# Kernel tuning notes

Hardware: AMD Instinct MI355X
Metric: run time of the kernel (lower is better)

## Reference

```python
import jax, jax.numpy as jnp
import numpy as np

# ---- constants matching init opt ----
SQRT_FRAGS = 8
N_PATCH = SQRT_FRAGS * SQRT_FRAGS  # 64
TH1_INIT = 0.85
PATCH_MEAN = 0.1
MORPH = 5          # morphology_size (odd -> same-size pooling)
STEP = 5e-5
FRAME_PATCHES = np.array([0, 1, 2, 3, 4, 5, 6, 7, 8, 15, 16, 23, 24, 31, 32, 39,
                          40, 47, 48, 55, 56, 57, 58, 59, 60, 61, 62, 63])
H = W = 3072


def setup_inputs() -> dict:
    key = jax.random.key(0)
    x = jax.random.uniform(key, (1, 1, H, W), dtype=jnp.float32)
    return {"x": x}


def _frac_above(p, th):
    # mean of where(p > th, 1, 0)
    return jnp.mean((p > th).astype(jnp.float32))


def _find_thresholds(patches):
    """Sequential per-patch threshold search with th1 carried across patches
    (faithful to the stateful self.th1 in the torch module).
    patches: (64, ph, pw). Returns per-patch final threshold (64,)."""
    f_bias = jnp.zeros((N_PATCH,), jnp.float32).at[jnp.asarray(FRAME_PATCHES)].set(0.05)

    def per_patch(th, inp):
        p, fb = inp
        lo_tgt = PATCH_MEAN + 0.02 - fb   # loop 1: while frac < lo_tgt: th -= STEP
        hi_tgt = PATCH_MEAN - 0.02 - fb   # loop 2: while frac > hi_tgt: th += STEP
        th = jax.lax.while_loop(lambda t: _frac_above(p, t) < lo_tgt,
                                lambda t: t - STEP, th)
        th = jax.lax.while_loop(lambda t: _frac_above(p, t) > hi_tgt,
                                lambda t: t + STEP, th)
        return th, th

    _, ths = jax.lax.scan(per_patch, jnp.float32(TH1_INIT), (patches, f_bias))
    return ths


def _maxpool(x, k=MORPH):
    # PyTorch MaxPool2d(k, stride=1, padding=k//2) pads with -inf -> same size
    pad = k // 2
    return jax.lax.reduce_window(
        x, -jnp.inf, jax.lax.max,
        window_dimensions=(1, 1, k, k), window_strides=(1, 1, 1, 1),
        padding=[(0, 0), (0, 0), (pad, pad), (pad, pad)])


def reference(x):
    N, c, h, w = x.shape
    ph, pw = h // SQRT_FRAGS, w // SQRT_FRAGS
    # unfold with kernel=stride=ph -> non-overlapping patches, row-major order
    patches = (x[0, 0]
               .reshape(SQRT_FRAGS, ph, SQRT_FRAGS, pw)
               .transpose(0, 2, 1, 3)
               .reshape(N_PATCH, ph, pw))
    ths = _find_thresholds(patches)
    binary = (patches > ths[:, None, None]).astype(jnp.float32)
    # fold back to full image
    img = (binary
           .reshape(SQRT_FRAGS, SQRT_FRAGS, ph, pw)
           .transpose(0, 2, 1, 3)
           .reshape(1, 1, h, w))
    # morphological close: maxpool then minpool (minpool = -maxpool(-x))
    out = -_maxpool(-_maxpool(img))
    return out
```

## Files before the change

### kernel.cpp

```cpp
#include <hip/hip_runtime.h>
#include <stdint.h>

constexpr int IMG     = 3072;
constexpr int NPIX    = IMG * IMG;
constexpr int PH      = 384;
constexpr int NPATCH  = 64;
constexpr int NSLICE  = 8;
constexpr int SROWS   = PH / NSLICE;
constexpr int WPR     = IMG / 32;
constexpr uint32_t KEY_LO = 0x3F000000u;
constexpr uint32_t STEPU = 839u;
constexpr uint32_t G0 = KEY_LO + 704u;
constexpr int NB = 9999;
constexpr int CH = (NB + 255) / 256;

constexpr int TR = 24;
constexpr int TC = 24;
constexpr int GR = IMG / TR;
constexpr int GC = WPR / TC;
constexpr int BROWS  = TR + 8;
constexpr int BWORDS = TC + 4;
constexpr int DROWS  = TR + 4;
constexpr int DWORDS = TC + 2;

constexpr size_t OFF_THS  = 0;
constexpr size_t OFF_PRIV = 512;

__global__ __launch_bounds__(256) void k_hist(const float* __restrict__ x,
                                              uint32_t* __restrict__ priv) {
    __shared__ uint32_t hist[NB];
    const int p = blockIdx.x >> 3, s = blockIdx.x & 7;
    const int t = threadIdx.x;
    const int pr = p >> 3, pc = p & 7;
    const float* base = x + (size_t)(pr * PH + s * SROWS) * IMG + pc * PH;

    for (int i = t; i < NB; i += 256) hist[i] = 0;
    __syncthreads();

    constexpr int NF4 = SROWS * (PH / 4);
    for (int i = t; i < NF4; i += 256) {
        int r = i / 96, c = i - r * 96;
        float4 v = *reinterpret_cast<const float4*>(base + (size_t)r * IMG + c * 4);
        float vals[4] = {v.x, v.y, v.z, v.w};
#pragma unroll
        for (int k = 0; k < 4; ++k) {
            uint32_t key = __float_as_uint(vals[k]);
            if (key > G0) {
                uint32_t idx = (key - KEY_LO + 134u) / 839u;
                if (idx > (uint32_t)(NB - 1)) idx = NB - 1;
                atomicAdd(&hist[idx], 1u);
            }
        }
    }
    __syncthreads();
    uint32_t* out = priv + (size_t)blockIdx.x * NB;
    for (int i = t; i < NB; i += 256) out[i] = hist[i];
}

__global__ __launch_bounds__(256) void k_scan(const uint32_t* __restrict__ priv,
                                              float* __restrict__ ths) {
    __shared__ uint32_t h[NB];
    __shared__ uint32_t csum[256];
    __shared__ uint32_t after[256];
    __shared__ int best_s[256];
    const int p = blockIdx.x, t = threadIdx.x;
    for (int i = t; i < NB; i += 256) {
        uint32_t sum = 0;
#pragma unroll
        for (int b = 0; b < NSLICE; ++b)
            sum += priv[(size_t)(p * NSLICE + b) * NB + i];
        h[i] = sum;
    }
    __syncthreads();

    const int lo = t * CH;
    const int hi = (lo + CH < NB) ? lo + CH : NB;
    uint32_t s = 0;
    for (int i = lo; i < hi; ++i) s += h[i];
    csum[t] = s;
    __syncthreads();
    if (t == 0) {
        uint32_t acc = 0;
        for (int u = 255; u >= 0; --u) { after[u] = acc; acc += csum[u]; }
    }
    __syncthreads();

    const int pr = p >> 3, pc = p & 7;
    const bool frame = (pr == 0 || pr == 7 || pc == 0 || pc == 7);
    const float hi_t = 0.08f - (frame ? 0.05f : 0.0f);
    int d = (int)((double)hi_t * 147456.0);
    while ((float)(d + 1) / 147456.0f <= hi_t) ++d;
    while (d > 0 && (float)d / 147456.0f > hi_t) --d;
    const uint32_t Chi = (uint32_t)d;

    uint32_t run = after[t];
    int best = 0x7FFFFFFF;
    for (int i = hi - 1; i >= lo; --i) {
        run += h[i];
        if (i >= 1 && run <= Chi) best = i;
    }
    best_s[t] = best;
    __syncthreads();
    for (int st = 128; st > 0; st >>= 1) {
        if (t < st) { int o = best_s[t + st]; if (o < best_s[t]) best_s[t] = o; }
        __syncthreads();
    }
    if (t == 0) {
        int istar = best_s[0];
        int j = (istar == 0x7FFFFFFF) ? (NB - 2) : (istar - 1);
        ths[p] = __uint_as_float(G0 + (uint32_t)j * STEPU);
    }
}

__device__ __forceinline__ uint32_t hshift5_or(uint32_t c, uint32_t l, uint32_t r) {
    uint64_t xr = ((uint64_t)r << 32) | c;
    uint64_t xl = ((uint64_t)c << 32) | l;
    return c | (uint32_t)(xr >> 1) | (uint32_t)(xr >> 2)
             | (uint32_t)(xl >> 31) | (uint32_t)(xl >> 30);
}
__device__ __forceinline__ uint32_t hshift5_and(uint32_t c, uint32_t l, uint32_t r) {
    uint64_t xr = ((uint64_t)r << 32) | c;
    uint64_t xl = ((uint64_t)c << 32) | l;
    return c & (uint32_t)(xr >> 1) & (uint32_t)(xr >> 2)
             & (uint32_t)(xl >> 31) & (uint32_t)(xl >> 30);
}

__global__ __launch_bounds__(256) void k_binclose(const float* __restrict__ x,
                                                  const float* __restrict__ ths,
                                                  float* __restrict__ out) {
    __shared__ float    ths_s[NPATCH];
    __shared__ uint32_t Bs[BROWS][BWORDS];
    __shared__ uint32_t Ds[DROWS][DWORDS];
    const int bid = blockIdx.x;
    const int ry = bid / GC, cx = bid - ry * GC;
    const int y0 = ry * TR;
    const int w0 = cx * TC;
    const int t = threadIdx.x;

    if (t < NPATCH) ths_s[t] = ths[t];
    __syncthreads();

    for (int i = t; i < BROWS * BWORDS; i += 256) {
        int r = i / BWORDS, w = i - r * BWORDS;
        int gy = y0 - 4 + r;
        int gw = w0 - 2 + w;
        uint32_t m = 0;
        if (gy >= 0 && gy < IMG && gw >= 0 && gw < WPR) {
            float th = ths_s[(gy / PH) * 8 + gw / 12];
            const float* row = x + (size_t)gy * IMG + gw * 32;
#pragma unroll
            for (int k = 0; k < 8; ++k) {
                float4 v = *reinterpret_cast<const float4*>(row + 4 * k);
                m |= (uint32_t)(v.x > th) << (4 * k + 0);
                m |= (uint32_t)(v.y > th) << (4 * k + 1);
                m |= (uint32_t)(v.z > th) << (4 * k + 2);
                m |= (uint32_t)(v.w > th) << (4 * k + 3);
            }
        }
        Bs[r][w] = m;
    }
    __syncthreads();

    for (int i = t; i < DROWS * DWORDS; i += 256) {
        int rd = i / DWORDS, wd = i - rd * DWORDS;
        uint32_t acc = 0;
#pragma unroll
        for (int dy = -2; dy <= 2; ++dy) {
            int rb = rd + 2 + dy;
            uint32_t cc = Bs[rb][wd + 1];
            uint32_t ll = Bs[rb][wd];
            uint32_t rr = Bs[rb][wd + 2];
            acc |= hshift5_or(cc, ll, rr);
        }
        Ds[rd][wd] = acc;
    }
    __syncthreads();

    for (int i = t; i < TR * TC; i += 256) {
        int r = i / TC, w = i - r * TC;
        int gy = y0 + r;
        int gw = w0 + w;
        uint32_t acc = 0xFFFFFFFFu;
#pragma unroll
        for (int dy = -2; dy <= 2; ++dy) {
            int yy = gy + dy;
            if (yy < 0 || yy >= IMG) continue;
            int rd = r + 2 + dy;
            uint32_t cc = Ds[rd][w + 1];
            uint32_t ll = (gw > 0)       ? Ds[rd][w]     : 0xFFFFFFFFu;
            uint32_t rr = (gw < WPR - 1) ? Ds[rd][w + 2] : 0xFFFFFFFFu;
            acc &= hshift5_and(cc, ll, rr);
        }
        float* o = out + (size_t)gy * IMG + gw * 32;
#pragma unroll
        for (int k = 0; k < 8; ++k) {
            float4 v;
            v.x = (acc & (1u << (4 * k + 0))) ? 1.0f : 0.0f;
            v.y = (acc & (1u << (4 * k + 1))) ? 1.0f : 0.0f;
            v.z = (acc & (1u << (4 * k + 2))) ? 1.0f : 0.0f;
            v.w = (acc & (1u << (4 * k + 3))) ? 1.0f : 0.0f;
            *reinterpret_cast<float4*>(o + 4 * k) = v;
        }
    }
}

extern "C" void kernel_launch(void* const* d_in, const int* in_sizes, int n_in,
                              void* d_out, int out_size, void* d_ws, size_t ws_size,
                              hipStream_t stream) {
    const float* x = (const float*)d_in[0];
    float* out = (float*)d_out;
    uint8_t* ws = (uint8_t*)d_ws;

    float*    ths  = (float*)(ws + OFF_THS);
    uint32_t* priv = (uint32_t*)(ws + OFF_PRIV);

    k_hist    <<<NPATCH * NSLICE, 256, 0, stream>>>(x, priv);
    k_scan    <<<NPATCH,          256, 0, stream>>>(priv, ths);
    k_binclose<<<GR * GC,         256, 0, stream>>>(x, ths, out);
}
```

Measured before the change: 135.4 us.

## Fuse histogram merge and threshold scan into hist kernel via last-block election

Removes the separate scan kernel. Each histogram block now writes its partial counts packed as 16-bit pairs, and the last-arriving slice block for each patch, detected with an atomic counter, merges the slices and computes the threshold. A memset resets the counters before each launch. The close kernel's tile width also doubles from 24 to 48 words, halving its block count. This trades a kernel launch and half the partial-histogram traffic for threadfence/atomic synchronisation and a serial tail on the elected blocks.

```diff
diff --git a/kernel.cpp b/kernel.cpp
--- a/kernel.cpp
+++ b/kernel.cpp
@@ -2,7 +2,6 @@
 #include <stdint.h>
 
 constexpr int IMG     = 3072;
-constexpr int NPIX    = IMG * IMG;
 constexpr int PH      = 384;
 constexpr int NPATCH  = 64;
 constexpr int NSLICE  = 8;
@@ -12,10 +11,12 @@
 constexpr uint32_t STEPU = 839u;
 constexpr uint32_t G0 = KEY_LO + 704u;
 constexpr int NB = 9999;
+constexpr int NPAIR    = 5000;
+constexpr int PRSTRIDE = 10000;
 constexpr int CH = (NB + 255) / 256;
 
 constexpr int TR = 24;
-constexpr int TC = 24;
+constexpr int TC = 48;
 constexpr int GR = IMG / TR;
 constexpr int GC = WPR / TC;
 constexpr int BROWS  = TR + 8;
@@ -24,17 +25,24 @@
 constexpr int DWORDS = TC + 2;
 
 constexpr size_t OFF_THS  = 0;
+constexpr size_t OFF_DONE = 256;
 constexpr size_t OFF_PRIV = 512;
 
 __global__ __launch_bounds__(256) void k_hist(const float* __restrict__ x,
-                                              uint32_t* __restrict__ priv) {
-    __shared__ uint32_t hist[NB];
+                                              uint16_t* __restrict__ priv,
+                                              uint32_t* __restrict__ done,
+                                              float* __restrict__ ths) {
+    __shared__ uint32_t hist[NB + 1];
+    __shared__ uint32_t csum[256];
+    __shared__ uint32_t after[256];
+    __shared__ int best_s[256];
+    __shared__ int elect_s;
     const int p = blockIdx.x >> 3, s = blockIdx.x & 7;
     const int t = threadIdx.x;
     const int pr = p >> 3, pc = p & 7;
     const float* base = x + (size_t)(pr * PH + s * SROWS) * IMG + pc * PH;
 
-    for (int i = t; i < NB; i += 256) hist[i] = 0;
+    for (int i = t; i < NB + 1; i += 256) hist[i] = 0;
     __syncthreads();
 
     constexpr int NF4 = SROWS * (PH / 4);
@@ -53,31 +61,48 @@
         }
     }
     __syncthreads();
-    uint32_t* out = priv + (size_t)blockIdx.x * NB;
-    for (int i = t; i < NB; i += 256) out[i] = hist[i];
-}
-
-__global__ __launch_bounds__(256) void k_scan(const uint32_t* __restrict__ priv,
-                                              float* __restrict__ ths) {
-    __shared__ uint32_t h[NB];
-    __shared__ uint32_t csum[256];
-    __shared__ uint32_t after[256];
-    __shared__ int best_s[256];
-    const int p = blockIdx.x, t = threadIdx.x;
-    for (int i = t; i < NB; i += 256) {
+
+    uint32_t* out = reinterpret_cast<uint32_t*>(priv + (size_t)blockIdx.x * PRSTRIDE);
+    for (int i = t; i < NPAIR; i += 256)
+        out[i] = (hist[2 * i] & 0xFFFFu) | (hist[2 * i + 1] << 16);
+
+    __syncthreads();
+    __threadfence();
+    __syncthreads();
+    if (t == 0) {
+        uint32_t old = atomicAdd(&done[p], 1u);
+        elect_s = (old == NSLICE - 1);
+    }
+    __syncthreads();
+    if (!elect_s) return;
+    __threadfence();
+
+    {
+        const uint32_t* rows[NSLICE];
+#pragma unroll
+        for (int b = 0; b < NSLICE; ++b)
+            rows[b] = reinterpret_cast<const uint32_t*>(priv + (size_t)(p * NSLICE + b) * PRSTRIDE);
+        for (int i = t; i < NPAIR; i += 256) {
+            uint32_t lo = 0, hi = 0;
+#pragma unroll
+            for (int b = 0; b < NSLICE; ++b) {
+                uint32_t v = rows[b][i];
+                lo += v & 0xFFFFu;
+                hi += v >> 16;
+            }
+            hist[2 * i]     = lo;
+            hist[2 * i + 1] = hi;
+        }
+    }
+    __syncthreads();
+
+    const int lo_i = t * CH;
+    const int hi_i = (lo_i + CH < NB) ? lo_i + CH : NB;
+    {
         uint32_t sum = 0;
-#pragma unroll
-        for (int b = 0; b < NSLICE; ++b)
-            sum += priv[(size_t)(p * NSLICE + b) * NB + i];
-        h[i] = sum;
-    }
-    __syncthreads();
-
-    const int lo = t * CH;
-    const int hi = (lo + CH < NB) ? lo + CH : NB;
-    uint32_t s = 0;
-    for (int i = lo; i < hi; ++i) s += h[i];
-    csum[t] = s;
+        for (int i = lo_i; i < hi_i; ++i) sum += hist[i];
+        csum[t] = sum;
+    }
     __syncthreads();
     if (t == 0) {
         uint32_t acc = 0;
@@ -85,7 +110,6 @@
     }
     __syncthreads();
 
-    const int pr = p >> 3, pc = p & 7;
     const bool frame = (pr == 0 || pr == 7 || pc == 0 || pc == 7);
     const float hi_t = 0.08f - (frame ? 0.05f : 0.0f);
     int d = (int)((double)hi_t * 147456.0);
@@ -93,13 +117,15 @@
     while (d > 0 && (float)d / 147456.0f > hi_t) --d;
     const uint32_t Chi = (uint32_t)d;
 
-    uint32_t run = after[t];
-    int best = 0x7FFFFFFF;
-    for (int i = hi - 1; i >= lo; --i) {
-        run += h[i];
-        if (i >= 1 && run <= Chi) best = i;
-    }
-    best_s[t] = best;
+    {
+        uint32_t run = after[t];
+        int best = 0x7FFFFFFF;
+        for (int i = hi_i - 1; i >= lo_i; --i) {
+            run += hist[i];
+            if (i >= 1 && run <= Chi) best = i;
+        }
+        best_s[t] = best;
+    }
     __syncthreads();
     for (int st = 128; st > 0; st >>= 1) {
         if (t < st) { int o = best_s[t + st]; if (o < best_s[t]) best_s[t] = o; }
@@ -212,9 +238,10 @@
     uint8_t* ws = (uint8_t*)d_ws;
 
     float*    ths  = (float*)(ws + OFF_THS);
-    uint32_t* priv = (uint32_t*)(ws + OFF_PRIV);
-
-    k_hist    <<<NPATCH * NSLICE, 256, 0, stream>>>(x, priv);
-    k_scan    <<<NPATCH,          256, 0, stream>>>(priv, ths);
+    uint32_t* done = (uint32_t*)(ws + OFF_DONE);
+    uint16_t* priv = (uint16_t*)(ws + OFF_PRIV);
+
+    hipMemsetAsync(done, 0, NPATCH * sizeof(uint32_t), stream);
+    k_hist    <<<NPATCH * NSLICE, 256, 0, stream>>>(x, priv, done, ths);
     k_binclose<<<GR * GC,         256, 0, stream>>>(x, ths, out);
 }
```

New measurement: 211.2 us. +55.9%, slower.
